# Kernel tuning notes

Hardware: AMD Instinct MI355X
Metric: run time of the kernel (lower is better)

Reference implementation:

```python
import jax, jax.numpy as jnp
import numpy as np

NEG = -9e15
ALPHA = 0.2  # leaky relu slope

def setup_inputs() -> dict:
    key = jax.random.key(0)
    k1, k2, k3, k4 = jax.random.split(key, 4)
    N, Fin, Fout = 8192, 512, 256
    h = jax.random.normal(k1, (N, Fin), dtype=jnp.float32)
    adj = jax.random.randint(k2, (N, N), 0, 2, dtype=jnp.int32)
    # xavier_uniform with gain=1.414
    gain = 1.414
    limW = gain * np.sqrt(6.0 / (Fin + Fout))
    W = jax.random.uniform(k3, (Fin, Fout), dtype=jnp.float32, minval=-limW, maxval=limW)
    lima = gain * np.sqrt(6.0 / (2 * Fout + 1))
    a = jax.random.uniform(k4, (2 * Fout, 1), dtype=jnp.float32, minval=-lima, maxval=lima)
    return {"h": h, "adj": adj, "W": W, "a": a}

def reference(h, adj, W, a):
    Fout = W.shape[1]
    Wh = h @ W                                   # [N, Fout]
    # decompose a = [a1; a2]: e_ij = leaky(a1.Wh_i + a2.Wh_j)
    f1 = Wh @ a[:Fout]                           # [N, 1]
    f2 = Wh @ a[Fout:]                           # [N, 1]
    e = jax.nn.leaky_relu(f1 + f2.T, negative_slope=ALPHA)  # [N, N]
    e = jnp.where(adj > 0, e, jnp.float32(NEG))
    attention = jax.nn.softmax(e, axis=1)
    # dropout is identity at inference (training=False)
    h_prime = attention @ Wh                     # [N, Fout]
    return jax.nn.elu(h_prime)
```

## Files before the change

kernel.cpp:

```cpp
#include <hip/hip_runtime.h>
#include <cstdint>
#include <cstddef>

#define ALPHA 0.2f

typedef __attribute__((ext_vector_type(8)))  short short8;
typedef __attribute__((ext_vector_type(16))) float f32x16;

static __device__ __forceinline__ unsigned short f2bf(float x) {
  union { float f; unsigned u; } c; c.f = x;
  unsigned u = c.u;
  unsigned r = (u + 0x7FFFu + ((u >> 16) & 1u)) >> 16;
  return (unsigned short)r;
}

__global__ __launch_bounds__(256, 2) void maskgemm(const int* __restrict__ adj,
                                                   unsigned long long* __restrict__ mask,
                                                   const float* __restrict__ h,
                                                   const float* __restrict__ W,
                                                   float* __restrict__ Wh) {
  __shared__ float As[32][68];
  __shared__ float Bs[32][64];
  __shared__ unsigned long long mbuf[4][128];
  const int t = threadIdx.x;
  const int b = blockIdx.x;
  if (b % 5 == 0) {
    const int bid = b / 5;
    const int nb = bid & 3, mb = bid >> 2;
    const int m0 = mb * 64, n0 = nb * 64;
    const int ty = t >> 4, tx = t & 15;
    float acc[4][4];
#pragma unroll
    for (int i = 0; i < 4; i++)
#pragma unroll
      for (int j = 0; j < 4; j++) acc[i][j] = 0.f;

    for (int k0 = 0; k0 < 512; k0 += 32) {
#pragma unroll
      for (int c = 0; c < 2; c++) {
        int m = c * 32 + (t >> 3);
        int kq = (t & 7) * 4;
        float4 v = *(const float4*)&h[(size_t)(m0 + m) * 512 + k0 + kq];
        As[kq + 0][m] = v.x; As[kq + 1][m] = v.y;
        As[kq + 2][m] = v.z; As[kq + 3][m] = v.w;
      }
#pragma unroll
      for (int c = 0; c < 2; c++) {
        int k = c * 16 + (t >> 4);
        int n = (t & 15) * 4;
        *(float4*)&Bs[k][n] = *(const float4*)&W[(size_t)(k0 + k) * 256 + n0 + n];
      }
      __syncthreads();
#pragma unroll
      for (int k = 0; k < 32; k++) {
        float4 a = *(float4*)&As[k][ty * 4];
        float4 bb = *(float4*)&Bs[k][tx * 4];
        float av[4] = {a.x, a.y, a.z, a.w};
        float bv[4] = {bb.x, bb.y, bb.z, bb.w};
#pragma unroll
        for (int i = 0; i < 4; i++)
#pragma unroll
          for (int j = 0; j < 4; j++) acc[i][j] = fmaf(av[i], bv[j], acc[i][j]);
      }
      __syncthreads();
    }
#pragma unroll
    for (int i = 0; i < 4; i++) {
      float4 v = {acc[i][0], acc[i][1], acc[i][2], acc[i][3]};
      *(float4*)&Wh[(size_t)(m0 + ty * 4 + i) * 256 + n0 + tx * 4] = v;
    }
  } else {
    const int mask_id = b - b / 5 - 1;
    const int wave = t >> 6, lane = t & 63;
    const int row = mask_id * 4 + wave;
    const int* ap = adj + (size_t)row * 8192 + lane;
#pragma unroll 1
    for (int it0 = 0; it0 < 128; it0 += 4) {
      int a0 = ap[(it0 + 0) * 64];
      int a1 = ap[(it0 + 1) * 64];
      int a2 = ap[(it0 + 2) * 64];
      int a3 = ap[(it0 + 3) * 64];
      unsigned long long b0 = __ballot(a0 > 0);
      unsigned long long b1 = __ballot(a1 > 0);
      unsigned long long b2 = __ballot(a2 > 0);
      unsigned long long b3 = __ballot(a3 > 0);
      if (lane == 0) {
        mbuf[wave][it0 + 0] = b0; mbuf[wave][it0 + 1] = b1;
        mbuf[wave][it0 + 2] = b2; mbuf[wave][it0 + 3] = b3;
      }
    }
    __syncthreads();
    uint4* dst = (uint4*)(mask + (size_t)mask_id * 4 * 128);
    dst[t] = ((const uint4*)mbuf)[t];
  }
}

__global__ __launch_bounds__(256) void rowstats(const float* __restrict__ Wh,
                                                const float* __restrict__ a,
                                                float* __restrict__ f1,
                                                float* __restrict__ f2,
                                                unsigned* __restrict__ uvpack) {
  const int t = threadIdx.x;
  const int w = t >> 6, lane = t & 63;
  const int i = blockIdx.x * 4 + w;
  float4 wv = *(const float4*)&Wh[(size_t)i * 256 + lane * 4];
  float4 a1 = *(const float4*)&a[lane * 4];
  float4 a2 = *(const float4*)&a[256 + lane * 4];
  float s1 = wv.x * a1.x + wv.y * a1.y + wv.z * a1.z + wv.w * a1.w;
  float s2 = wv.x * a2.x + wv.y * a2.y + wv.z * a2.z + wv.w * a2.w;
#pragma unroll
  for (int off = 32; off; off >>= 1) { s1 += __shfl_xor(s1, off); s2 += __shfl_xor(s2, off); }
  if (lane == 0) {
    f1[i] = s1; f2[i] = s2;
    float u = __expf(s2), v = __expf(ALPHA * s2);
    uvpack[i] = (unsigned)f2bf(u) | ((unsigned)f2bf(v) << 16);
  }
}

__global__ __launch_bounds__(256) void wtrans(const float* __restrict__ Wh,
                                              unsigned short* __restrict__ WhT) {
  __shared__ unsigned short T[64][80];
  const int t = threadIdx.x;
  const int bi = blockIdx.x & 127;
  const int bc = blockIdx.x >> 7;
  const int i0 = bi * 64, c0 = bc * 64;
  {
    const int il = t >> 2, cq = (t & 3) * 16;
#pragma unroll
    for (int k = 0; k < 4; ++k) {
      float4 v = *(const float4*)&Wh[(size_t)(i0 + il) * 256 + c0 + cq + k * 4];
      T[cq + k * 4 + 0][il] = f2bf(v.x);
      T[cq + k * 4 + 1][il] = f2bf(v.y);
      T[cq + k * 4 + 2][il] = f2bf(v.z);
      T[cq + k * 4 + 3][il] = f2bf(v.w);
    }
  }
  __syncthreads();
  {
    const int cl = t >> 2, iq = (t & 3) * 16;
    *(uint4*)&WhT[(size_t)(c0 + cl) * 8192 + i0 + iq]     = *(const uint4*)&T[cl][iq];
    *(uint4*)&WhT[(size_t)(c0 + cl) * 8192 + i0 + iq + 8] = *(const uint4*)&T[cl][iq + 8];
  }
}

__global__ __launch_bounds__(256) void f2max_k(const float* __restrict__ f2,
                                               float* __restrict__ f2maxp) {
  __shared__ float red[256];
  const int t = threadIdx.x;
  float m = -1e30f;
  for (int c = 0; c < 32; c++) m = fmaxf(m, f2[c * 256 + t]);
  red[t] = m;
  __syncthreads();
  for (int s = 128; s; s >>= 1) {
    if (t < s) red[t] = fmaxf(red[t], red[t + s]);
    __syncthreads();
  }
  if (t == 0) f2maxp[0] = red[0];
}

#define LOADBF(BUF, SIDX)                                                        \
  {                                                                              \
    const int s_ = (SIDX) < 128 ? (SIDX) : 127;                                  \
    BUF[0] = *(const short8*)(wtp0 + (size_t)0 * (32 * 8192) + (size_t)s_ * 16); \
    BUF[1] = *(const short8*)(wtp0 + (size_t)1 * (32 * 8192) + (size_t)s_ * 16); \
    BUF[2] = *(const short8*)(wtp0 + (size_t)2 * (32 * 8192) + (size_t)s_ * 16); \
    BUF[3] = *(const short8*)(wtp0 + (size_t)3 * (32 * 8192) + (size_t)s_ * 16); \
  }

#define ATTN_SUB(KSUB, MWORD, UCA, UCB, BFC)                                     \
  {                                                                              \
    const unsigned mbyte_ = ((MWORD) >> (((KSUB) & 1) * 16 + aselsh)) & 0xFFu;   \
    const unsigned uu_[8] = {UCA.x, UCA.y, UCA.z, UCA.w, UCB.x, UCB.y, UCB.z, UCB.w}; \
    float w_[8];                                                                 \
    _Pragma("unroll")                                                            \
    for (int jj = 0; jj < 8; jj++) {                                             \
      union { unsigned u; float f; } cu_, cv_;                                   \
      cu_.u = uu_[jj] << 16;                                                     \
      cv_.u = uu_[jj] & 0xFFFF0000u;                                             \
      float wv_ = (cu_.f > Ui) ? Ai * cu_.f : Bi * cv_.f;                        \
      int ext_ = ((int)(mbyte_ << (31 - jj))) >> 31;    \
      union { float f; int i; } wu_; wu_.f = wv_; wu_.i &= ext_;                 \
      w_[jj] = wu_.f;                                                            \
    }                                                                            \
    lpriv += ((w_[0] + w_[1]) + (w_[2] + w_[3])) + ((w_[4] + w_[5]) + (w_[6] + w_[7])); \
    union { uint4 q; short8 s; } af_;                                            \
    asm("v_cvt_pk_bf16_f32 %0, %1, %2" : "=v"(af_.q.x) : "v"(w_[0]), "v"(w_[1]));\
    asm("v_cvt_pk_bf16_f32 %0, %1, %2" : "=v"(af_.q.y) : "v"(w_[2]), "v"(w_[3]));\
    asm("v_cvt_pk_bf16_f32 %0, %1, %2" : "=v"(af_.q.z) : "v"(w_[4]), "v"(w_[5]));\
    asm("v_cvt_pk_bf16_f32 %0, %1, %2" : "=v"(af_.q.w) : "v"(w_[6]), "v"(w_[7]));\
    acc[0] = __builtin_amdgcn_mfma_f32_32x32x16_bf16(af_.s, BFC[0], acc[0], 0, 0, 0); \
    acc[1] = __builtin_amdgcn_mfma_f32_32x32x16_bf16(af_.s, BFC[1], acc[1], 0, 0, 0); \
    acc[2] = __builtin_amdgcn_mfma_f32_32x32x16_bf16(af_.s, BFC[2], acc[2], 0, 0, 0); \
    acc[3] = __builtin_amdgcn_mfma_f32_32x32x16_bf16(af_.s, BFC[3], acc[3], 0, 0, 0); \
  }

#define ATTN_GROUP(G, UC, UN, MC, MN)                                            \
  {                                                                              \
    const int gn_ = (G) < 31 ? (G) + 1 : 31;                                     \
    MN = mp[gn_];                                                                \
    UN[0] = *(const uint4*)(uvp + gn_ * 64 + 0);                                 \
    UN[1] = *(const uint4*)(uvp + gn_ * 64 + 4);                                 \
    LOADBF(bfs2, 4 * (G) + 2);             \
    LOADBF(bfs3, 4 * (G) + 3);                                                   \
    ATTN_SUB(0, MC.x, UC[0], UC[1], bfs0);                                       \
    UN[2] = *(const uint4*)(uvp + gn_ * 64 + 16);                                \
    UN[3] = *(const uint4*)(uvp + gn_ * 64 + 20);                                \
    ATTN_SUB(1, MC.x, UC[2], UC[3], bfs1);                                       \
    UN[4] = *(const uint4*)(uvp + gn_ * 64 + 32);                                \
    UN[5] = *(const uint4*)(uvp + gn_ * 64 + 36);                                \
    LOADBF(bfs0, 4 * (G) + 4);             \
    LOADBF(bfs1, 4 * (G) + 5);                                                   \
    ATTN_SUB(2, MC.y, UC[4], UC[5], bfs2);                                       \
    UN[6] = *(const uint4*)(uvp + gn_ * 64 + 48);                                \
    UN[7] = *(const uint4*)(uvp + gn_ * 64 + 52);                                \
    ATTN_SUB(3, MC.y, UC[6], UC[7], bfs3);                                       \
  }

__global__ __launch_bounds__(256, 1) void attn_main(const unsigned long long* __restrict__ maskw,
                                                    const float* __restrict__ f1,
                                                    const unsigned* __restrict__ uvpack,
                                                    const unsigned short* __restrict__ WhT,
                                                    const float* __restrict__ f2maxp,
                                                    float* __restrict__ out) {
  __shared__ float red[4][32][132];
  __shared__ float lsum[4][32];
  const int t = threadIdx.x;
  const int wave = t >> 6, lane = t & 63;
  const int jq = wave;
  const int am = lane & 31, asel = lane >> 5;
  const int aselsh = asel * 8;
  const int bid = blockIdx.x;
  const int cg = bid & 1;
  const int r0 = (bid >> 1) * 32;
  const int row = r0 + am;

  const float F2max = f2maxp[0];
  const float f1v = f1[row];
  const float x = f1v + F2max;
  const float M = x > 0.f ? x : ALPHA * x;
  const float Ai = __expf(f1v - M);
  const float Bi = __expf(ALPHA * f1v - M);
  const float Ui = __expf(-f1v);

  f32x16 acc[4] = {};
  const uint2* mp = (const uint2*)maskw + (size_t)row * 128 + jq * 32;
  const unsigned* uvp = uvpack + jq * 2048 + aselsh;
  const unsigned short* wtp0 = WhT + (size_t)(cg * 128 + am) * 8192 + jq * 2048 + aselsh;

  uint2 mg = mp[0], mgN;
  uint4 ug[8], ugN[8];
#pragma unroll
  for (int k = 0; k < 4; k++) {
    ug[2 * k]     = *(const uint4*)(uvp + k * 16);
    ug[2 * k + 1] = *(const uint4*)(uvp + k * 16 + 4);
  }
  short8 bfs0[4], bfs1[4], bfs2[4], bfs3[4];
  LOADBF(bfs0, 0);
  LOADBF(bfs1, 1);
  float lpriv = 0.f;

#pragma unroll 1
  for (int gg = 0; gg < 16; ++gg) {
    ATTN_GROUP(2 * gg,     ug,  ugN, mg,  mgN);
    ATTN_GROUP(2 * gg + 1, ugN, ug,  mgN, mg);
  }

#pragma unroll
  for (int ct = 0; ct < 4; ct++) {
#pragma unroll
    for (int reg = 0; reg < 16; reg++) {
      const int rowl = (reg & 3) + 8 * (reg >> 2) + 4 * asel;
      red[jq][rowl][ct * 32 + am] = acc[ct][reg];
    }
  }
  lpriv += __shfl_xor(lpriv, 32);
  if (asel == 0) lsum[jq][am] = lpriv;
  __syncthreads();

  const int rr = t >> 3, cb = (t & 7) * 16;
  const float l = lsum[0][rr] + lsum[1][rr] + lsum[2][rr] + lsum[3][rr];
  const float inv = 1.0f / fmaxf(l, 1e-30f);
#pragma unroll
  for (int cc = 0; cc < 16; cc += 4) {
    float4 v;
    v.x = red[0][rr][cb + cc + 0] + red[1][rr][cb + cc + 0] + red[2][rr][cb + cc + 0] + red[3][rr][cb + cc + 0];
    v.y = red[0][rr][cb + cc + 1] + red[1][rr][cb + cc + 1] + red[2][rr][cb + cc + 1] + red[3][rr][cb + cc + 1];
    v.z = red[0][rr][cb + cc + 2] + red[1][rr][cb + cc + 2] + red[2][rr][cb + cc + 2] + red[3][rr][cb + cc + 2];
    v.w = red[0][rr][cb + cc + 3] + red[1][rr][cb + cc + 3] + red[2][rr][cb + cc + 3] + red[3][rr][cb + cc + 3];
    v.x *= inv; v.y *= inv; v.z *= inv; v.w *= inv;
    float4 o;
    o.x = v.x > 0.f ? v.x : __expf(v.x) - 1.f;
    o.y = v.y > 0.f ? v.y : __expf(v.y) - 1.f;
    o.z = v.z > 0.f ? v.z : __expf(v.z) - 1.f;
    o.w = v.w > 0.f ? v.w : __expf(v.w) - 1.f;
    *(float4*)&out[(size_t)(r0 + rr) * 256 + cg * 128 + cb + cc] = o;
  }
}

extern "C" void kernel_launch(void* const* d_in, const int* in_sizes, int n_in,
                              void* d_out, int out_size, void* d_ws, size_t ws_size,
                              hipStream_t stream) {
  const float* h  = (const float*)d_in[0];
  const int* adj  = (const int*)d_in[1];
  const float* W  = (const float*)d_in[2];
  const float* a  = (const float*)d_in[3];
  float* out = (float*)d_out;
  char* ws = (char*)d_ws;

  float* Wh            = (float*)ws;
  unsigned long long* mask = (unsigned long long*)(ws + (size_t)(8u << 20));
  unsigned short* WhT  = (unsigned short*)(ws + (size_t)(16u << 20));
  float* f1            = (float*)(ws + (size_t)(20u << 20));
  float* f2            = (float*)(ws + (size_t)(20u << 20) + (32u << 10));
  unsigned* uvpack     = (unsigned*)(ws + (size_t)(20u << 20) + (64u << 10));
  float* f2maxp        = (float*)(ws + (size_t)(20u << 20) + (96u << 10));

  maskgemm<<<2560, 256, 0, stream>>>(adj, mask, h, W, Wh);
  rowstats<<<2048, 256, 0, stream>>>(Wh, a, f1, f2, uvpack);
  wtrans<<<512, 256, 0, stream>>>(Wh, WhT);
  f2max_k<<<1, 256, 0, stream>>>(f2, f2maxp);
  attn_main<<<512, 256, 0, stream>>>(mask, f1, uvpack, WhT, f2maxp, out);
}
```

Before: 537.4 us.

## Pre-pack Wh into MFMA fragment layout and transpose mask storage

Replaces the row-major bf16 transpose of Wh with a pack kernel that writes each 32-column by 16-k slab in exact MFMA B-fragment order, so each lane in attn_main loads contiguous 16-byte chunks. The mask is stored column-group-major so the 32 rows of a block read adjacent 8-byte words per group. The goal is fully coalesced global loads in the main attention loop. The cost is that the pack kernel runs with only 128 blocks and does strided scalar reads of Wh, and the mask writes in maskgemm become scattered.

Result: faster. 468.9 us (-12.8%).

```diff
diff --git a/kernel.cpp b/kernel.cpp
--- a/kernel.cpp
+++ b/kernel.cpp
@@ -90,8 +90,10 @@
       }
     }
     __syncthreads();
-    uint4* dst = (uint4*)(mask + (size_t)mask_id * 4 * 128);
-    dst[t] = ((const uint4*)mbuf)[t];
+    const int it = t & 127, half = t >> 7;
+    const int row0 = mask_id * 4;
+    unsigned long long tmp[2] = {mbuf[half * 2][it], mbuf[half * 2 + 1][it]};
+    *(uint4*)&mask[(size_t)it * 8192 + row0 + half * 2] = *(const uint4*)tmp;
   }
 }
 
@@ -117,29 +119,19 @@
   }
 }
 
-__global__ __launch_bounds__(256) void wtrans(const float* __restrict__ Wh,
-                                              unsigned short* __restrict__ WhT) {
-  __shared__ unsigned short T[64][80];
-  const int t = threadIdx.x;
-  const int bi = blockIdx.x & 127;
-  const int bc = blockIdx.x >> 7;
-  const int i0 = bi * 64, c0 = bc * 64;
-  {
-    const int il = t >> 2, cq = (t & 3) * 16;
-#pragma unroll
-    for (int k = 0; k < 4; ++k) {
-      float4 v = *(const float4*)&Wh[(size_t)(i0 + il) * 256 + c0 + cq + k * 4];
-      T[cq + k * 4 + 0][il] = f2bf(v.x);
-      T[cq + k * 4 + 1][il] = f2bf(v.y);
-      T[cq + k * 4 + 2][il] = f2bf(v.z);
-      T[cq + k * 4 + 3][il] = f2bf(v.w);
-    }
-  }
-  __syncthreads();
-  {
-    const int cl = t >> 2, iq = (t & 3) * 16;
-    *(uint4*)&WhT[(size_t)(c0 + cl) * 8192 + i0 + iq]     = *(const uint4*)&T[cl][iq];
-    *(uint4*)&WhT[(size_t)(c0 + cl) * 8192 + i0 + iq + 8] = *(const uint4*)&T[cl][iq + 8];
+__global__ __launch_bounds__(256) void bpack(const float* __restrict__ Wh,
+                                             unsigned short* __restrict__ BP) {
+  const int t = threadIdx.x, wave = t >> 6, lane = t & 63;
+  const int c32 = blockIdx.x >> 4, sblk = blockIdx.x & 15;
+  const int col = c32 * 32 + (lane & 31), hi = lane >> 5;
+#pragma unroll
+  for (int p = 0; p < 8; p++) {
+    const int s = sblk * 32 + wave * 8 + p;
+    unsigned short v[8];
+#pragma unroll
+    for (int e = 0; e < 8; e++)
+      v[e] = f2bf(Wh[(size_t)(s * 16 + hi * 8 + e) * 256 + col]);
+    *(uint4*)&BP[((size_t)c32 * 512 + s) * 512 + lane * 8] = *(const uint4*)v;
   }
 }
 
@@ -161,10 +153,10 @@
 #define LOADBF(BUF, SIDX)                                                        \
   {                                                                              \
     const int s_ = (SIDX) < 128 ? (SIDX) : 127;                                  \
-    BUF[0] = *(const short8*)(wtp0 + (size_t)0 * (32 * 8192) + (size_t)s_ * 16); \
-    BUF[1] = *(const short8*)(wtp0 + (size_t)1 * (32 * 8192) + (size_t)s_ * 16); \
-    BUF[2] = *(const short8*)(wtp0 + (size_t)2 * (32 * 8192) + (size_t)s_ * 16); \
-    BUF[3] = *(const short8*)(wtp0 + (size_t)3 * (32 * 8192) + (size_t)s_ * 16); \
+    BUF[0] = *(const short8*)(bp0 + (size_t)(0 * 512 + s_) * 512);               \
+    BUF[1] = *(const short8*)(bp0 + (size_t)(1 * 512 + s_) * 512);               \
+    BUF[2] = *(const short8*)(bp0 + (size_t)(2 * 512 + s_) * 512);               \
+    BUF[3] = *(const short8*)(bp0 + (size_t)(3 * 512 + s_) * 512);               \
   }
 
 #define ATTN_SUB(KSUB, MWORD, UCA, UCB, BFC)                                     \
@@ -197,7 +189,7 @@
 #define ATTN_GROUP(G, UC, UN, MC, MN)                                            \
   {                                                                              \
     const int gn_ = (G) < 31 ? (G) + 1 : 31;                                     \
-    MN = mp[gn_];                                                                \
+    MN = mp[(size_t)gn_ * 8192];                                                 \
     UN[0] = *(const uint4*)(uvp + gn_ * 64 + 0);                                 \
     UN[1] = *(const uint4*)(uvp + gn_ * 64 + 4);                                 \
     LOADBF(bfs2, 4 * (G) + 2);             \
@@ -219,7 +211,7 @@
 __global__ __launch_bounds__(256, 1) void attn_main(const unsigned long long* __restrict__ maskw,
                                                     const float* __restrict__ f1,
                                                     const unsigned* __restrict__ uvpack,
-                                                    const unsigned short* __restrict__ WhT,
+                                                    const unsigned short* __restrict__ BP,
                                                     const float* __restrict__ f2maxp,
                                                     float* __restrict__ out) {
   __shared__ float red[4][32][132];
@@ -243,9 +235,9 @@
   const float Ui = __expf(-f1v);
 
   f32x16 acc[4] = {};
-  const uint2* mp = (const uint2*)maskw + (size_t)row * 128 + jq * 32;
+  const uint2* mp = (const uint2*)maskw + (size_t)(jq * 32) * 8192 + row;
   const unsigned* uvp = uvpack + jq * 2048 + aselsh;
-  const unsigned short* wtp0 = WhT + (size_t)(cg * 128 + am) * 8192 + jq * 2048 + aselsh;
+  const unsigned short* bp0 = BP + ((size_t)(cg * 4) * 512 + jq * 128) * 512 + lane * 8;
 
   uint2 mg = mp[0], mgN;
   uint4 ug[8], ugN[8];
@@ -309,7 +301,7 @@
 
   float* Wh            = (float*)ws;
   unsigned long long* mask = (unsigned long long*)(ws + (size_t)(8u << 20));
-  unsigned short* WhT  = (unsigned short*)(ws + (size_t)(16u << 20));
+  unsigned short* BP   = (unsigned short*)(ws + (size_t)(16u << 20));
   float* f1            = (float*)(ws + (size_t)(20u << 20));
   float* f2            = (float*)(ws + (size_t)(20u << 20) + (32u << 10));
   unsigned* uvpack     = (unsigned*)(ws + (size_t)(20u << 20) + (64u << 10));
@@ -317,7 +309,7 @@
 
   maskgemm<<<2560, 256, 0, stream>>>(adj, mask, h, W, Wh);
   rowstats<<<2048, 256, 0, stream>>>(Wh, a, f1, f2, uvpack);
-  wtrans<<<512, 256, 0, stream>>>(Wh, WhT);
+  bpack<<<128, 256, 0, stream>>>(Wh, BP);
   f2max_k<<<1, 256, 0, stream>>>(f2, f2maxp);
-  attn_main<<<512, 256, 0, stream>>>(mask, f1, uvpack, WhT, f2maxp, out);
-}
+  attn_main<<<512, 256, 0, stream>>>(mask, f1, uvpack, BP, f2maxp, out);
+}
```
